# Optimization experiments

Hardware: AMD Instinct MI355X
Metric: run time of the kernel (lower is better)

Reference implementation:

```python
import jax, jax.numpy as jnp
import numpy as np

N_HEAD, D_HEAD, D_MODEL = 16, 64, 1024
QLEN, MLEN, BSZ = 512, 512, 8
KLEN = QLEN + MLEN
SCALE = 1.0 / D_HEAD ** 0.5
LN_EPS = 1e-5


def rel_shift(x):
    # x: [qlen, klen, bsz, n_head] -- Transformer-XL pad/reshape shift trick
    q, k, b, n = x.shape
    x_pad = jnp.pad(x, ((0, 0), (1, 0), (0, 0), (0, 0)))
    x_pad = x_pad.reshape(k + 1, q, b, n)
    return x_pad[1:].reshape(q, k, b, n)


def setup_inputs() -> dict:
    key = jax.random.key(0)
    ks = jax.random.split(key, 10)
    s = 0.02
    return {
        'w': jax.random.normal(ks[0], (QLEN, BSZ, D_MODEL), jnp.float32),
        'r': jax.random.normal(ks[1], (KLEN, D_MODEL), jnp.float32),
        'mems': jax.random.normal(ks[2], (MLEN, BSZ, D_MODEL), jnp.float32),
        'r_w_bias': jax.random.normal(ks[3], (N_HEAD, D_HEAD), jnp.float32) * s,
        'r_r_bias': jax.random.normal(ks[4], (N_HEAD, D_HEAD), jnp.float32) * s,
        'Wq': jax.random.normal(ks[5], (N_HEAD * D_HEAD, D_MODEL), jnp.float32) * s,
        'Wkv': jax.random.normal(ks[6], (2 * N_HEAD * D_HEAD, D_MODEL), jnp.float32) * s,
        'Wr': jax.random.normal(ks[7], (N_HEAD * D_HEAD, D_MODEL), jnp.float32) * s,
        'br': jnp.zeros((N_HEAD * D_HEAD,), jnp.float32),
        'Wo': jax.random.normal(ks[8], (D_MODEL, N_HEAD * D_HEAD), jnp.float32) * s,
        'bo': jnp.zeros((D_MODEL,), jnp.float32),
        'gamma': jnp.ones((D_MODEL,), jnp.float32),
        'beta': jnp.zeros((D_MODEL,), jnp.float32),
    }


def reference(w, r, mems, r_w_bias, r_r_bias, Wq, Wkv, Wr, br, Wo, bo, gamma, beta):
    qlen, bsz, _ = w.shape
    cat = jnp.concatenate([mems, w], axis=0)           # [klen, b, d]
    klen = cat.shape[0]
    mlen = klen - qlen

    q = (w @ Wq.T).reshape(qlen, bsz, N_HEAD, D_HEAD)   # [i, b, n, d]
    kv = (cat @ Wkv.T).reshape(klen, bsz, N_HEAD, 2 * D_HEAD)
    k, v = kv[..., :D_HEAD], kv[..., D_HEAD:]           # [j, b, n, d]
    rk = (r @ Wr.T + br).reshape(klen, N_HEAD, D_HEAD)  # [j, n, d]

    AC = jnp.einsum('ibnd,jbnd->ijbn', q + r_w_bias, k)
    BD = jnp.einsum('ibnd,jnd->ijbn', q + r_r_bias, rk)
    BD = rel_shift(BD)
    score = (AC + BD) * SCALE                           # [i, j, b, n]

    # causal mask with memory: query i attends to keys j <= i + mlen
    i_idx = jnp.arange(qlen)[:, None]
    j_idx = jnp.arange(klen)[None, :]
    mask = j_idx > (i_idx + mlen)
    score = jnp.where(mask[:, :, None, None], -1e30, score)

    prob = jax.nn.softmax(score, axis=1)
    attn_vec = jnp.einsum('ijbn,jbnd->ibnd', prob, v).reshape(qlen, bsz, N_HEAD * D_HEAD)
    attn_out = attn_vec @ Wo.T + bo

    # IdentityResidualGate: x + relu(y), then LayerNorm
    y = w + jax.nn.relu(attn_out)
    mu = jnp.mean(y, axis=-1, keepdims=True)
    var = jnp.mean(jnp.square(y - mu), axis=-1, keepdims=True)
    return (y - mu) * jax.lax.rsqrt(var + LN_EPS) * gamma + beta
```

## Files before the change

kernel.cpp:

```cpp
#include <hip/hip_runtime.h>
#include <hip/hip_bf16.h>
#include <cstdint>
#include <cstddef>

typedef __attribute__((ext_vector_type(4))) float f32x4;
typedef __attribute__((ext_vector_type(8))) short bf16x8;
using u16 = unsigned short;

#define ATT_SCALE 0.125f

__device__ __forceinline__ u16 f2b(float f) {
    union { float f; uint32_t u; } x; x.f = f;
    uint32_t r = x.u + 0x7fffu + ((x.u >> 16) & 1u);
    return (u16)(r >> 16);
}
__device__ __forceinline__ float b2f(u16 u) {
    union { uint32_t u; float f; } x; x.u = (uint32_t)u << 16; return x.f;
}

#define GLDS16(g, s)                                                        \
    __builtin_amdgcn_global_load_lds(                                       \
        (const __attribute__((address_space(1))) uint32_t*)(g),             \
        (__attribute__((address_space(3))) uint32_t*)(s), 16, 0, 0)

__global__ __launch_bounds__(256) void prep_kernel(
    const float* __restrict__ mems, const float* __restrict__ w,
    const float* __restrict__ r, const float* __restrict__ Wq,
    const float* __restrict__ Wkv, const float* __restrict__ Wr,
    const float* __restrict__ Wo, u16* __restrict__ cat_b,
    u16* __restrict__ r_b, u16* __restrict__ Wq_b, u16* __restrict__ Wkv_b,
    u16* __restrict__ Wr_b, u16* __restrict__ Wo_b) {
    int bid = blockIdx.x;
    if (bid < 8192) {
        int col4 = threadIdx.x;
        float4 v;
        int b, oj;
        if (bid < 4096) {
            v = reinterpret_cast<const float4*>(mems)[(size_t)bid * 256 + col4];
            b = bid & 7; oj = bid >> 3;
        } else {
            int rrow = bid - 4096;
            v = reinterpret_cast<const float4*>(w)[(size_t)rrow * 256 + col4];
            b = rrow & 7; oj = 512 + (rrow >> 3);
        }
        uint2 o;
        o.x = (uint32_t)f2b(v.x) | ((uint32_t)f2b(v.y) << 16);
        o.y = (uint32_t)f2b(v.z) | ((uint32_t)f2b(v.w) << 16);
        reinterpret_cast<uint2*>(cat_b)[(size_t)(b * 1024 + oj) * 256 + col4] = o;
        return;
    }
    bid -= 8192;
    const float4* src;
    uint2* dst;
    if (bid < 1024)      { src = (const float4*)r;   dst = (uint2*)r_b; }
    else if (bid < 2048) { src = (const float4*)Wq;  dst = (uint2*)Wq_b;  bid -= 1024; }
    else if (bid < 4096) { src = (const float4*)Wkv; dst = (uint2*)Wkv_b; bid -= 2048; }
    else if (bid < 5120) { src = (const float4*)Wr;  dst = (uint2*)Wr_b;  bid -= 4096; }
    else                 { src = (const float4*)Wo;  dst = (uint2*)Wo_b;  bid -= 5120; }
    int idx = bid * 256 + threadIdx.x;
    float4 v = src[idx];
    uint2 o;
    o.x = (uint32_t)f2b(v.x) | ((uint32_t)f2b(v.y) << 16);
    o.y = (uint32_t)f2b(v.z) | ((uint32_t)f2b(v.w) << 16);
    dst[idx] = o;
}

__global__ __launch_bounds__(512, 1) void kv_gemm(const u16* __restrict__ catb,
                                                  const u16* __restrict__ Wkvb,
                                                  u16* __restrict__ kb,
                                                  u16* __restrict__ vtb) {
    __shared__ u16 sA[2][256][64];
    __shared__ u16 sB[2][256][64];
    const int tid = threadIdx.x;
    const int wid = tid >> 6, lane = tid & 63;
    const int lr = lane & 15, lg = lane >> 4;
    const int bm = blockIdx.x * 256, bn = blockIdx.y * 256;
    const int Wm = (wid >> 2) * 128, Wn = (wid & 3) * 64;
    const int srow = tid >> 3, scol = tid & 7;
    const int xs = lr & 7;
    const u16* A = catb + (size_t)bm * 1024;
    const u16* B = Wkvb + (size_t)bn * 1024;
    f32x4 acc[8][4] = {};

#pragma unroll
    for (int p = 0; p < 4; p++) {
        int row = p * 64 + srow;
        int cs = (scol ^ (row & 7)) * 8;
        GLDS16(A + (size_t)row * 1024 + cs, &sA[0][row][scol * 8]);
        GLDS16(B + (size_t)row * 1024 + cs, &sB[0][row][scol * 8]);
    }
    __syncthreads();

    int cur = 0;
    for (int t = 0; t < 16; t++) {
        if (t < 15) {
            const int k0n = (t + 1) * 64;
#pragma unroll
            for (int p = 0; p < 4; p++) {
                int row = p * 64 + srow;
                int cs = (scol ^ (row & 7)) * 8;
                GLDS16(A + (size_t)row * 1024 + k0n + cs, &sA[cur ^ 1][row][scol * 8]);
                GLDS16(B + (size_t)row * 1024 + k0n + cs, &sB[cur ^ 1][row][scol * 8]);
            }
        }
#pragma unroll
        for (int ks = 0; ks < 2; ks++) {
            bf16x8 af[8], bfr[4];
#pragma unroll
            for (int mi = 0; mi < 8; mi++)
                af[mi] = *reinterpret_cast<const bf16x8*>(
                    &sA[cur][Wm + mi * 16 + lr][((ks * 4 + lg) ^ xs) * 8]);
#pragma unroll
            for (int ni = 0; ni < 4; ni++)
                bfr[ni] = *reinterpret_cast<const bf16x8*>(
                    &sB[cur][Wn + ni * 16 + lr][((ks * 4 + lg) ^ xs) * 8]);
#pragma unroll
            for (int mi = 0; mi < 8; mi++)
#pragma unroll
                for (int ni = 0; ni < 4; ni++)
                    acc[mi][ni] = __builtin_amdgcn_mfma_f32_16x16x32_bf16(
                        af[mi], bfr[ni], acc[mi][ni], 0, 0, 0);
        }
        __syncthreads();
        cur ^= 1;
    }
#pragma unroll
    for (int mi = 0; mi < 8; mi++)
#pragma unroll
        for (int ni = 0; ni < 4; ni++) {
            const int m0 = bm + Wm + mi * 16 + lg * 4;
            const int c = bn + Wn + ni * 16 + lr;
            const int b = m0 >> 10, j0 = m0 & 1023;
            const int n = c >> 7, dd = c & 127;
            if (dd < 64) {
#pragma unroll
                for (int rr = 0; rr < 4; rr++)
                    kb[(((size_t)(b * 16 + n)) * 1024 + j0 + rr) * 64 + dd] =
                        f2b(acc[mi][ni][rr]);
            } else {
                uint2 pk;
                pk.x = (uint32_t)f2b(acc[mi][ni][0]) | ((uint32_t)f2b(acc[mi][ni][1]) << 16);
                pk.y = (uint32_t)f2b(acc[mi][ni][2]) | ((uint32_t)f2b(acc[mi][ni][3]) << 16);
                *reinterpret_cast<uint2*>(
                    vtb + (((size_t)(b * 16 + n)) * 64 + (dd - 64)) * 1024 + j0) = pk;
            }
        }
}

__global__ __launch_bounds__(256, 2) void qr_gemm(
    const u16* __restrict__ catb, const u16* __restrict__ Wqb,
    const u16* __restrict__ rb, const u16* __restrict__ Wrb,
    const float* __restrict__ bw, const float* __restrict__ brr,
    const float* __restrict__ br, u16* __restrict__ qwb,
    u16* __restrict__ qrb, u16* __restrict__ rkb) {
    __shared__ u16 sA[2][128][64];
    __shared__ u16 sB[2][128][64];
    const int idx = blockIdx.x;
    const u16 *A, *B;
    int bx, by, epi;
    if (idx < 256) {
        epi = 0; B = Wqb; bx = idx & 31; by = idx >> 5;
        int bm0 = bx * 128;
        A = catb + ((size_t)(bm0 >> 9) * 1024 + 512 + (bm0 & 511)) * 1024;
    } else {
        epi = 2; B = Wrb;
        int l = idx - 256; bx = l & 7; by = l >> 3;
        A = rb + (size_t)bx * 128 * 1024;
    }
    const int tid = threadIdx.x;
    const int wid = tid >> 6, lane = tid & 63;
    const int lr = lane & 15, lg = lane >> 4;
    const int bm = bx * 128, bn = by * 128;
    const int wm = (wid >> 1) * 64, wn = (wid & 1) * 64;
    const int srow = tid >> 3, scol = tid & 7;
    f32x4 acc[4][4] = {};

#pragma unroll
    for (int p = 0; p < 4; p++) {
        int row = p * 32 + srow;
        GLDS16(A + (size_t)row * 1024 + scol * 8, &sA[0][row][scol * 8]);
        GLDS16(B + (size_t)(bn + row) * 1024 + scol * 8, &sB[0][row][scol * 8]);
    }
    __syncthreads();

    int cur = 0;
    for (int t = 0; t < 16; t++) {
        if (t < 15) {
            const int k0n = (t + 1) * 64;
#pragma unroll
            for (int p = 0; p < 4; p++) {
                int row = p * 32 + srow;
                GLDS16(A + (size_t)row * 1024 + k0n + scol * 8, &sA[cur ^ 1][row][scol * 8]);
                GLDS16(B + (size_t)(bn + row) * 1024 + k0n + scol * 8,
                       &sB[cur ^ 1][row][scol * 8]);
            }
        }
#pragma unroll
        for (int ks = 0; ks < 2; ks++) {
            bf16x8 af[4], bfr[4];
#pragma unroll
            for (int x = 0; x < 4; x++) {
                af[x] = *reinterpret_cast<const bf16x8*>(
                    &sA[cur][wm + x * 16 + lr][(ks * 4 + lg) * 8]);
                bfr[x] = *reinterpret_cast<const bf16x8*>(
                    &sB[cur][wn + x * 16 + lr][(ks * 4 + lg) * 8]);
            }
#pragma unroll
            for (int mi = 0; mi < 4; mi++)
#pragma unroll
                for (int ni = 0; ni < 4; ni++)
                    acc[mi][ni] = __builtin_amdgcn_mfma_f32_16x16x32_bf16(
                        af[mi], bfr[ni], acc[mi][ni], 0, 0, 0);
        }
        __syncthreads();
        cur ^= 1;
    }
#pragma unroll
    for (int mi = 0; mi < 4; mi++)
#pragma unroll
        for (int ni = 0; ni < 4; ni++) {
            const int m0 = bm + wm + mi * 16 + lg * 4;
            const int c = bn + wn + ni * 16 + lr;
            if (epi == 0) {
#pragma unroll
                for (int rr = 0; rr < 4; rr++) {
                    int m = m0 + rr;
                    qwb[(size_t)m * 1024 + c] = f2b(acc[mi][ni][rr] + bw[c]);
                    qrb[(size_t)m * 1024 + c] = f2b(acc[mi][ni][rr] + brr[c]);
                }
            } else {
                const int nh = c >> 6, d = c & 63;
#pragma unroll
                for (int rr = 0; rr < 4; rr++)
                    rkb[((size_t)nh * 1024 + m0 + rr) * 64 + d] = f2b(acc[mi][ni][rr] + br[c]);
            }
        }
}

__global__ __launch_bounds__(256, 2) void gemm_out(const u16* __restrict__ A,
                                                   const u16* __restrict__ B,
                                                   const float* __restrict__ wres,
                                                   const float* __restrict__ bo,
                                                   float* __restrict__ y) {
    __shared__ u16 sA[2][128][64];
    __shared__ u16 sB[2][128][64];
    const int tid = threadIdx.x;
    const int wid = tid >> 6, lane = tid & 63;
    const int lr = lane & 15, lg = lane >> 4;
    const int bm = blockIdx.x * 128, bn = blockIdx.y * 128;
    const int wm = (wid >> 1) * 64, wn = (wid & 1) * 64;
    const int srow = tid >> 3, scol = tid & 7;
    f32x4 acc[4][4] = {};

#pragma unroll
    for (int p = 0; p < 4; p++) {
        int row = p * 32 + srow;
        GLDS16(A + (size_t)(bm + row) * 1024 + scol * 8, &sA[0][row][scol * 8]);
        GLDS16(B + (size_t)(bn + row) * 1024 + scol * 8, &sB[0][row][scol * 8]);
    }
    __syncthreads();

    int cur = 0;
    for (int t = 0; t < 16; t++) {
        if (t < 15) {
            const int k0n = (t + 1) * 64;
#pragma unroll
            for (int p = 0; p < 4; p++) {
                int row = p * 32 + srow;
                GLDS16(A + (size_t)(bm + row) * 1024 + k0n + scol * 8,
                       &sA[cur ^ 1][row][scol * 8]);
                GLDS16(B + (size_t)(bn + row) * 1024 + k0n + scol * 8,
                       &sB[cur ^ 1][row][scol * 8]);
            }
        }
#pragma unroll
        for (int ks = 0; ks < 2; ks++) {
            bf16x8 af[4], bfr[4];
#pragma unroll
            for (int x = 0; x < 4; x++) {
                af[x] = *reinterpret_cast<const bf16x8*>(
                    &sA[cur][wm + x * 16 + lr][(ks * 4 + lg) * 8]);
                bfr[x] = *reinterpret_cast<const bf16x8*>(
                    &sB[cur][wn + x * 16 + lr][(ks * 4 + lg) * 8]);
            }
#pragma unroll
            for (int mi = 0; mi < 4; mi++)
#pragma unroll
                for (int ni = 0; ni < 4; ni++)
                    acc[mi][ni] = __builtin_amdgcn_mfma_f32_16x16x32_bf16(
                        af[mi], bfr[ni], acc[mi][ni], 0, 0, 0);
        }
        __syncthreads();
        cur ^= 1;
    }
#pragma unroll
    for (int mi = 0; mi < 4; mi++)
#pragma unroll
        for (int ni = 0; ni < 4; ni++)
#pragma unroll
            for (int rr = 0; rr < 4; rr++) {
                int m = bm + wm + mi * 16 + lg * 4 + rr;
                int c = bn + wn + ni * 16 + lr;
                y[(size_t)m * 1024 + c] =
                    wres[(size_t)m * 1024 + c] + fmaxf(acc[mi][ni][rr] + bo[c], 0.0f);
            }
}

__global__ __launch_bounds__(256, 3) void attn_kernel(const u16* __restrict__ qw,
                                                      const u16* __restrict__ qr,
                                                      const u16* __restrict__ kbuf,
                                                      const u16* __restrict__ vt,
                                                      const u16* __restrict__ rkb,
                                                      u16* __restrict__ attnv) {
    __shared__ uint4 ksh[64][8];
    __shared__ uint4 vsh[64][8];
    __shared__ uint4 rsh[128][8];
    __shared__ u16 bds[4][16][82];
    __shared__ u16 ps[4][16][72];
    const int bid = blockIdx.x;
    const int wg = (bid & 7) * 128 + (bid >> 3);
    const int i0 = (wg & 7) * 64;
    const int bnid = wg >> 3;
    const int b = bnid & 7, n = bnid >> 3;
    const int tid = threadIdx.x, wid = tid >> 6, lane = tid & 63;
    const int lr = lane & 15, lg = lane >> 4;
    const int it = i0 + wid * 16;

    const u16* qwp = qw + ((size_t)(b * 512 + it + lr)) * 1024 + n * 64;
    const u16* qrp = qr + ((size_t)(b * 512 + it + lr)) * 1024 + n * 64;
    bf16x8 aqw[2], aqr[2];
#pragma unroll
    for (int ks = 0; ks < 2; ks++) {
        aqw[ks] = *reinterpret_cast<const bf16x8*>(qwp + (ks * 4 + lg) * 8);
        aqr[ks] = *reinterpret_cast<const bf16x8*>(qrp + (ks * 4 + lg) * 8);
    }
    const u16* kp = kbuf + ((size_t)(b * 16 + n)) * 65536;
    const u16* vp = vt + ((size_t)(b * 16 + n)) * 65536;
    const u16* rp = rkb + (size_t)n * 65536;

    f32x4 acc[4] = {};
    float lpart[4] = {0.f, 0.f, 0.f, 0.f};
    const int xs = lr & 7;
    const int rbase = 48 - 16 * wid;

    const int nt = (i0 + 639) >> 6;
    for (int t = 0; t < nt; t++) {
        const int j0 = t << 6;
        const int jrb = j0 + 448 - i0;
#pragma unroll
        for (int inst = 0; inst < 2; inst++) {
            int gi = wid * 128 + inst * 64 + lane;
            int row = gi >> 3, c = gi & 7;
            int cs = (c ^ (row & 7)) * 8;
            GLDS16(kp + (size_t)(j0 + row) * 64 + cs,
                   (char*)ksh + (size_t)(wid * 128 + inst * 64) * 16);
            GLDS16(vp + (size_t)row * 1024 + j0 + cs,
                   (char*)vsh + (size_t)(wid * 128 + inst * 64) * 16);
        }
#pragma unroll
        for (int inst = 0; inst < 4; inst++) {
            int gi = wid * 256 + inst * 64 + lane;
            int row = gi >> 3, c = gi & 7;
            int grow = jrb + row;
            if (grow > 1023) grow = 1023;
            GLDS16(rp + (size_t)grow * 64 + (c ^ (row & 7)) * 8,
                   (char*)rsh + (size_t)(wid * 256 + inst * 64) * 16);
        }
        __syncthreads();

        f32x4 s[4] = {};
#pragma unroll
        for (int fj = 0; fj < 4; fj++)
#pragma unroll
            for (int ks = 0; ks < 2; ks++) {
                bf16x8 bk = *reinterpret_cast<const bf16x8*>(
                    &ksh[fj * 16 + lr][(ks * 4 + lg) ^ xs]);
                s[fj] = __builtin_amdgcn_mfma_f32_16x16x32_bf16(aqw[ks], bk, s[fj], 0, 0, 0);
            }
        f32x4 bd[5] = {};
#pragma unroll
        for (int fb = 0; fb < 5; fb++) {
            int rel = rbase + fb * 16 + lr;
#pragma unroll
            for (int ks = 0; ks < 2; ks++) {
                bf16x8 brk = *reinterpret_cast<const bf16x8*>(
                    &rsh[rel][(ks * 4 + lg) ^ xs]);
                bd[fb] = __builtin_amdgcn_mfma_f32_16x16x32_bf16(aqr[ks], brk, bd[fb], 0, 0, 0);
            }
        }
#pragma unroll
        for (int fb = 0; fb < 5; fb++)
#pragma unroll
            for (int rr = 0; rr < 4; rr++)
                bds[wid][lg * 4 + rr][fb * 16 + lr] = f2b(bd[fb][rr]);

#pragma unroll
        for (int fj = 0; fj < 4; fj++)
#pragma unroll
            for (int rr = 0; rr < 4; rr++) {
                const int di = lg * 4 + rr;
                float v = (s[fj][rr] + b2f(bds[wid][di][fj * 16 + lr + 15 - di])) * ATT_SCALE;
                float e = (j0 + fj * 16 + lr <= it + di + 512) ? __expf(v) : 0.0f;
                lpart[rr] += e;
                ps[wid][di][fj * 16 + lr] = f2b(e);
            }
#pragma unroll
        for (int kc = 0; kc < 2; kc++) {
            bf16x8 ap = *reinterpret_cast<const bf16x8*>(&ps[wid][lr][kc * 32 + lg * 8]);
#pragma unroll
            for (int nd = 0; nd < 4; nd++) {
                bf16x8 bv = *reinterpret_cast<const bf16x8*>(
                    &vsh[nd * 16 + lr][(kc * 4 + lg) ^ xs]);
                acc[nd] = __builtin_amdgcn_mfma_f32_16x16x32_bf16(ap, bv, acc[nd], 0, 0, 0);
            }
        }
        __syncthreads();
    }
    float l[4];
#pragma unroll
    for (int rr = 0; rr < 4; rr++) {
        float x = lpart[rr];
        x += __shfl_xor(x, 1);
        x += __shfl_xor(x, 2);
        x += __shfl_xor(x, 4);
        x += __shfl_xor(x, 8);
        l[rr] = x;
    }
#pragma unroll
    for (int nd = 0; nd < 4; nd++)
#pragma unroll
        for (int rr = 0; rr < 4; rr++) {
            int i = it + lg * 4 + rr;
            int d = nd * 16 + lr;
            attnv[((size_t)i * 8 + b) * 1024 + n * 64 + d] = f2b(acc[nd][rr] / l[rr]);
        }
}

__global__ __launch_bounds__(256) void ln_kernel(const float* __restrict__ y,
                                                 const float* __restrict__ gamma,
                                                 const float* __restrict__ beta,
                                                 float* __restrict__ out) {
    __shared__ float rs[8];
    int row = blockIdx.x, tid = threadIdx.x;
    const float4 v = reinterpret_cast<const float4*>(y + (size_t)row * 1024)[tid];
    float s = v.x + v.y + v.z + v.w;
    float s2 = v.x * v.x + v.y * v.y + v.z * v.z + v.w * v.w;
#pragma unroll
    for (int m = 1; m < 64; m <<= 1) {
        s += __shfl_xor(s, m);
        s2 += __shfl_xor(s2, m);
    }
    if ((tid & 63) == 0) {
        rs[tid >> 6] = s;
        rs[4 + (tid >> 6)] = s2;
    }
    __syncthreads();
    s = rs[0] + rs[1] + rs[2] + rs[3];
    s2 = rs[4] + rs[5] + rs[6] + rs[7];
    float mu = s * (1.0f / 1024.0f);
    float var = s2 * (1.0f / 1024.0f) - mu * mu;
    float inv = rsqrtf(var + 1e-5f);
    float4 g = reinterpret_cast<const float4*>(gamma)[tid];
    float4 be = reinterpret_cast<const float4*>(beta)[tid];
    float4 o;
    o.x = (v.x - mu) * inv * g.x + be.x;
    o.y = (v.y - mu) * inv * g.y + be.y;
    o.z = (v.z - mu) * inv * g.z + be.z;
    o.w = (v.w - mu) * inv * g.w + be.w;
    reinterpret_cast<float4*>(out + (size_t)row * 1024)[tid] = o;
}

extern "C" void kernel_launch(void* const* d_in, const int* in_sizes, int n_in,
                              void* d_out, int out_size, void* d_ws, size_t ws_size,
                              hipStream_t stream) {
    (void)in_sizes; (void)n_in; (void)out_size; (void)ws_size;
    const float* w_in  = (const float*)d_in[0];
    const float* r_in  = (const float*)d_in[1];
    const float* mems  = (const float*)d_in[2];
    const float* bw    = (const float*)d_in[3];
    const float* brr   = (const float*)d_in[4];
    const float* Wq    = (const float*)d_in[5];
    const float* Wkv   = (const float*)d_in[6];
    const float* Wr    = (const float*)d_in[7];
    const float* br    = (const float*)d_in[8];
    const float* Wo    = (const float*)d_in[9];
    const float* bo    = (const float*)d_in[10];
    const float* gamma = (const float*)d_in[11];
    const float* beta  = (const float*)d_in[12];

    char* base = (char*)d_ws;
    size_t off = 0;
    auto alloc = [&](size_t bytes) -> char* {
        char* p = base + off;
        off += (bytes + 255) & ~(size_t)255;
        return p;
    };
    u16* cat_b = (u16*)alloc((size_t)8192 * 1024 * 2);
    u16* r_b   = (u16*)alloc((size_t)1024 * 1024 * 2);
    u16* Wq_b  = (u16*)alloc((size_t)1024 * 1024 * 2);
    u16* Wkv_b = (u16*)alloc((size_t)2048 * 1024 * 2);
    u16* Wr_b  = (u16*)alloc((size_t)1024 * 1024 * 2);
    u16* Wo_b  = (u16*)alloc((size_t)1024 * 1024 * 2);
    u16* qw_b  = (u16*)alloc((size_t)4096 * 1024 * 2);
    u16* qr_b  = (u16*)alloc((size_t)4096 * 1024 * 2);
    u16* k_b   = (u16*)alloc((size_t)128 * 1024 * 64 * 2);
    u16* vt_b  = (u16*)alloc((size_t)128 * 64 * 1024 * 2);
    u16* rk_b  = (u16*)alloc((size_t)16 * 1024 * 64 * 2);
    u16* av_b  = (u16*)alloc((size_t)4096 * 1024 * 2);
    float* y = (float*)cat_b;

    prep_kernel<<<14336, 256, 0, stream>>>(mems, w_in, r_in, Wq, Wkv, Wr, Wo,
                                           cat_b, r_b, Wq_b, Wkv_b, Wr_b, Wo_b);

    kv_gemm<<<dim3(32, 8), 512, 0, stream>>>(cat_b, Wkv_b, k_b, vt_b);
    qr_gemm<<<320, 256, 0, stream>>>(cat_b, Wq_b, r_b, Wr_b, bw, brr, br,
                                     qw_b, qr_b, rk_b);

    attn_kernel<<<1024, 256, 0, stream>>>(qw_b, qr_b, k_b, vt_b, rk_b, av_b);

    gemm_out<<<dim3(32, 8), 256, 0, stream>>>(av_b, Wo_b, w_in, bo, y);

    ln_kernel<<<4096, 256, 0, stream>>>(y, gamma, beta, (float*)d_out);
}
```

Measured before the change: 204.6 us.

## Fold softmax scale into Q, store residual in bf16, add MFMA priority hints

Pre-multiplies the q projections by scale*log2(e) so the attention loop can use exp2f without a per-element multiply. Stores the pre-LayerNorm residual sum as bf16 instead of fp32, halving that intermediate's write and read traffic. Also reverses the block-to-i-tile ordering in attention and wraps the MFMA sections in s_setprio raise/lower. Storing the residual in bf16 loses precision before LayerNorm.

```diff
diff --git a/kernel.cpp b/kernel.cpp
--- a/kernel.cpp
+++ b/kernel.cpp
@@ -7,7 +7,7 @@
 typedef __attribute__((ext_vector_type(8))) short bf16x8;
 using u16 = unsigned short;
 
-#define ATT_SCALE 0.125f
+#define SCLOG2E 0.18033688011112043f
 
 __device__ __forceinline__ u16 f2b(float f) {
     union { float f; uint32_t u; } x; x.f = f;
@@ -225,8 +225,8 @@
 #pragma unroll
                 for (int rr = 0; rr < 4; rr++) {
                     int m = m0 + rr;
-                    qwb[(size_t)m * 1024 + c] = f2b(acc[mi][ni][rr] + bw[c]);
-                    qrb[(size_t)m * 1024 + c] = f2b(acc[mi][ni][rr] + brr[c]);
+                    qwb[(size_t)m * 1024 + c] = f2b((acc[mi][ni][rr] + bw[c]) * SCLOG2E);
+                    qrb[(size_t)m * 1024 + c] = f2b((acc[mi][ni][rr] + brr[c]) * SCLOG2E);
                 }
             } else {
                 const int nh = c >> 6, d = c & 63;
@@ -241,7 +241,7 @@
                                                    const u16* __restrict__ B,
                                                    const float* __restrict__ wres,
                                                    const float* __restrict__ bo,
-                                                   float* __restrict__ y) {
+                                                   u16* __restrict__ y) {
     __shared__ u16 sA[2][128][64];
     __shared__ u16 sB[2][128][64];
     const int tid = threadIdx.x;
@@ -301,8 +301,8 @@
             for (int rr = 0; rr < 4; rr++) {
                 int m = bm + wm + mi * 16 + lg * 4 + rr;
                 int c = bn + wn + ni * 16 + lr;
-                y[(size_t)m * 1024 + c] =
-                    wres[(size_t)m * 1024 + c] + fmaxf(acc[mi][ni][rr] + bo[c], 0.0f);
+                float v = wres[(size_t)m * 1024 + c] + fmaxf(acc[mi][ni][rr] + bo[c], 0.0f);
+                y[(size_t)m * 1024 + c] = f2b(v);
             }
 }
 
@@ -318,7 +318,7 @@
     __shared__ u16 bds[4][16][82];
     __shared__ u16 ps[4][16][72];
     const int bid = blockIdx.x;
-    const int wg = (bid & 7) * 128 + (bid >> 3);
+    const int wg = (bid & 7) * 128 + ((bid >> 3) ^ 7);
     const int i0 = (wg & 7) * 64;
     const int bnid = wg >> 3;
     const int b = bnid & 7, n = bnid >> 3;
@@ -368,6 +368,7 @@
         }
         __syncthreads();
 
+        __builtin_amdgcn_s_setprio(1);
         f32x4 s[4] = {};
 #pragma unroll
         for (int fj = 0; fj < 4; fj++)
@@ -388,6 +389,7 @@
                 bd[fb] = __builtin_amdgcn_mfma_f32_16x16x32_bf16(aqr[ks], brk, bd[fb], 0, 0, 0);
             }
         }
+        __builtin_amdgcn_s_setprio(0);
 #pragma unroll
         for (int fb = 0; fb < 5; fb++)
 #pragma unroll
@@ -399,11 +401,12 @@
 #pragma unroll
             for (int rr = 0; rr < 4; rr++) {
                 const int di = lg * 4 + rr;
-                float v = (s[fj][rr] + b2f(bds[wid][di][fj * 16 + lr + 15 - di])) * ATT_SCALE;
-                float e = (j0 + fj * 16 + lr <= it + di + 512) ? __expf(v) : 0.0f;
+                float v = s[fj][rr] + b2f(bds[wid][di][fj * 16 + lr + 15 - di]);
+                float e = (j0 + fj * 16 + lr <= it + di + 512) ? exp2f(v) : 0.0f;
                 lpart[rr] += e;
                 ps[wid][di][fj * 16 + lr] = f2b(e);
             }
+        __builtin_amdgcn_s_setprio(1);
 #pragma unroll
         for (int kc = 0; kc < 2; kc++) {
             bf16x8 ap = *reinterpret_cast<const bf16x8*>(&ps[wid][lr][kc * 32 + lg * 8]);
@@ -414,6 +417,7 @@
                 acc[nd] = __builtin_amdgcn_mfma_f32_16x16x32_bf16(ap, bv, acc[nd], 0, 0, 0);
             }
         }
+        __builtin_amdgcn_s_setprio(0);
         __syncthreads();
     }
     float l[4];
@@ -436,15 +440,16 @@
         }
 }
 
-__global__ __launch_bounds__(256) void ln_kernel(const float* __restrict__ y,
+__global__ __launch_bounds__(256) void ln_kernel(const u16* __restrict__ y,
                                                  const float* __restrict__ gamma,
                                                  const float* __restrict__ beta,
                                                  float* __restrict__ out) {
     __shared__ float rs[8];
     int row = blockIdx.x, tid = threadIdx.x;
-    const float4 v = reinterpret_cast<const float4*>(y + (size_t)row * 1024)[tid];
-    float s = v.x + v.y + v.z + v.w;
-    float s2 = v.x * v.x + v.y * v.y + v.z * v.z + v.w * v.w;
+    ushort4 u = reinterpret_cast<const ushort4*>(y + (size_t)row * 1024)[tid];
+    float v0 = b2f(u.x), v1 = b2f(u.y), v2 = b2f(u.z), v3 = b2f(u.w);
+    float s = v0 + v1 + v2 + v3;
+    float s2 = v0 * v0 + v1 * v1 + v2 * v2 + v3 * v3;
 #pragma unroll
     for (int m = 1; m < 64; m <<= 1) {
         s += __shfl_xor(s, m);
@@ -463,10 +468,10 @@
     float4 g = reinterpret_cast<const float4*>(gamma)[tid];
     float4 be = reinterpret_cast<const float4*>(beta)[tid];
     float4 o;
-    o.x = (v.x - mu) * inv * g.x + be.x;
-    o.y = (v.y - mu) * inv * g.y + be.y;
-    o.z = (v.z - mu) * inv * g.z + be.z;
-    o.w = (v.w - mu) * inv * g.w + be.w;
+    o.x = (v0 - mu) * inv * g.x + be.x;
+    o.y = (v1 - mu) * inv * g.y + be.y;
+    o.z = (v2 - mu) * inv * g.z + be.z;
+    o.w = (v3 - mu) * inv * g.w + be.w;
     reinterpret_cast<float4*>(out + (size_t)row * 1024)[tid] = o;
 }
 
@@ -507,7 +512,7 @@
     u16* vt_b  = (u16*)alloc((size_t)128 * 64 * 1024 * 2);
     u16* rk_b  = (u16*)alloc((size_t)16 * 1024 * 64 * 2);
     u16* av_b  = (u16*)alloc((size_t)4096 * 1024 * 2);
-    float* y = (float*)cat_b;
+    u16* y     = (u16*)cat_b;
 
     prep_kernel<<<14336, 256, 0, stream>>>(mems, w_in, r_in, Wq, Wkv, Wr, Wo,
                                            cat_b, r_b, Wq_b, Wkv_b, Wr_b, Wo_b);
```

New measurement: 202.5 us. About the same (-1.0%).
